# Kernel tuning notes

Hardware: AMD Instinct MI355X
Metric: run time of the kernel (lower is better)

## Reference

```python
import jax, jax.numpy as jnp
from jax import lax
import numpy as np

COMMITMENT_COST = 0.25
N_EMBED = 512
EDIM = 32


def _conv(x, w, b, stride, pad):
    # x: NCHW, w: OIHW (torch Conv2d layout)
    y = lax.conv_general_dilated(x, w, (stride, stride), [(pad, pad), (pad, pad)],
                                 dimension_numbers=("NCHW", "OIHW", "NCHW"))
    return y + b[None, :, None, None]


def _conv_t(x, w, b, stride, pad):
    # torch ConvTranspose2d weight layout: (in, out, kH, kW)
    k = w.shape[2]
    w_ = jnp.flip(w, (2, 3)).transpose(1, 0, 2, 3)  # -> OIHW
    p = k - 1 - pad
    y = lax.conv_general_dilated(x, w_, (1, 1), [(p, p), (p, p)],
                                 lhs_dilation=(stride, stride),
                                 dimension_numbers=("NCHW", "OIHW", "NCHW"))
    return y + b[None, :, None, None]


def setup_inputs() -> dict:
    key = jax.random.key(0)
    ks = jax.random.split(key, 9)
    rn = lambda k, s: jax.random.normal(k, s, jnp.float32) * 0.05
    return {
        "x": jax.random.normal(ks[0], (32, 3, 256, 256), jnp.float32),
        "e_w1": rn(ks[1], (64, 3, 4, 4)),    "e_b1": jnp.zeros((64,), jnp.float32),
        "e_w2": rn(ks[2], (128, 64, 4, 4)),  "e_b2": jnp.zeros((128,), jnp.float32),
        "e_w3": rn(ks[3], (32, 128, 3, 3)),  "e_b3": jnp.zeros((32,), jnp.float32),
        "embed": jax.random.uniform(ks[4], (N_EMBED, EDIM), jnp.float32,
                                    -1.0 / N_EMBED, 1.0 / N_EMBED),
        "d_w1": rn(ks[5], (32, 128, 3, 3)),  "d_b1": jnp.zeros((128,), jnp.float32),
        "d_w2": rn(ks[6], (128, 64, 4, 4)),  "d_b2": jnp.zeros((64,), jnp.float32),
        "d_w3": rn(ks[7], (64, 3, 4, 4)),    "d_b3": jnp.zeros((3,), jnp.float32),
    }


def reference(x, e_w1, e_b1, e_w2, e_b2, e_w3, e_b3, embed,
              d_w1, d_b1, d_w2, d_b2, d_w3, d_b3):
    # ---- encoder ----
    h = jax.nn.relu(_conv(x, e_w1, e_b1, 2, 1))   # [B,64,128,128]
    h = jax.nn.relu(_conv(h, e_w2, e_b2, 2, 1))   # [B,128,64,64]
    z = jax.nn.relu(_conv(h, e_w3, e_b3, 1, 1))   # [B,32,64,64]
    # ---- vector quantizer ----
    zp = z.transpose(0, 2, 3, 1)                  # BHWC
    zf = zp.reshape(-1, EDIM)                     # [N, 32]
    d = (zf ** 2).sum(1, keepdims=True) + (embed ** 2).sum(1) \
        - 2.0 * zf @ embed.T                      # [N, n_embed]
    idx = jnp.argmin(d, axis=1)                   # [N]
    z_q = embed[idx].reshape(zp.shape)            # gather == onehot @ embed
    sg = lax.stop_gradient
    loss = jnp.mean((sg(z_q) - zp) ** 2) + COMMITMENT_COST * jnp.mean((z_q - sg(zp)) ** 2)
    z_q_st = zp + sg(z_q - zp)                    # straight-through
    z_q_st = z_q_st.transpose(0, 3, 1, 2)         # back to NCHW
    # ---- decoder ----
    h = jax.nn.relu(_conv_t(z_q_st, d_w1, d_b1, 1, 1))  # [B,128,64,64]
    h = jax.nn.relu(_conv_t(h, d_w2, d_b2, 2, 1))       # [B,64,128,128]
    x_recon = _conv_t(h, d_w3, d_b3, 2, 1)              # [B,3,256,256]
    return x_recon, loss
```

## Files before the change

### kernel.cpp

```cpp
#include <hip/hip_runtime.h>


typedef __attribute__((ext_vector_type(8))) short     short8;
typedef __attribute__((ext_vector_type(4))) short     s16x4;
typedef __attribute__((ext_vector_type(8))) __bf16    bf16x8;
typedef __attribute__((ext_vector_type(4))) float     f32x4;
typedef __attribute__((ext_vector_type(4))) unsigned  uint32x4;

__device__ __forceinline__ float b2f(unsigned short b) {
  union { unsigned u; float f; } v; v.u = ((unsigned)b) << 16; return v.f;
}
__device__ __forceinline__ unsigned short f2b(float f) {
  union { float f; unsigned u; } v; v.f = f;
  unsigned r = v.u + 0x7FFF + ((v.u >> 16) & 1);
  return (unsigned short)(r >> 16);
}

__global__ __launch_bounds__(256) void prep1v_k(const float* __restrict__ w,
                                                unsigned short* __restrict__ wq) {
  const int i = blockIdx.x*256 + threadIdx.x;
  const int j = i & 7, l = (i >> 3) & 63, ni = (i >> 9) & 3, ks = i >> 11;
  const int k = ks*32 + (l >> 4)*8 + j;
  const int co = ni*16 + (l & 15);
  wq[i] = (k < 48) ? f2b(w[co*48 + k]) : (unsigned short)0;
}
__global__ __launch_bounds__(256) void prep2v_k(const float* __restrict__ w,
                                                unsigned short* __restrict__ wq) {
  const int i = blockIdx.x*256 + threadIdx.x;
  const int j = i & 7, l = (i >> 3) & 63, ni = (i >> 9) & 7, ks = i >> 12;
  const int lm = l & 15, lk = l >> 4;
  const int tap = ks >> 1, cc = ks & 1;
  const int co = ni*16 + lm, ci = cc*32 + lk*8 + j;
  wq[i] = f2b(w[(co*64 + ci)*16 + tap]);
}
__global__ __launch_bounds__(256) void prep3v_k(const float* __restrict__ w,
                                                unsigned short* __restrict__ wq) {
  const int i = blockIdx.x*256 + threadIdx.x;
  const int j = i & 7, l = (i >> 3) & 63, ni = (i >> 9) & 1, ks = i >> 10;
  const int lm = l & 15, lk = l >> 4;
  const int tap = ks >> 2, cf = ks & 3;
  const int co = ni*16 + lm, ci = cf*32 + lk*8 + j;
  wq[i] = f2b(w[(co*128 + ci)*9 + tap]);
}
__global__ __launch_bounds__(256) void prep4v_k(const float* __restrict__ w,
                                                unsigned short* __restrict__ wq) {
  const int i = blockIdx.x*256 + threadIdx.x;
  const int j = i & 7, l = (i >> 3) & 63, ni = (i >> 9) & 7, tap = i >> 12;
  const int lm = l & 15, lk = l >> 4;
  const int co = ni*16 + lm, ci = lk*8 + j;
  wq[i] = f2b(w[(ci*128 + co)*9 + (8 - tap)]);
}
__global__ __launch_bounds__(256) void prep5v_k(const float* __restrict__ w,
                                                unsigned short* __restrict__ wq) {
  const int i = blockIdx.x*256 + threadIdx.x;
  const int j = i & 7, l = (i >> 3) & 63, ni = (i >> 9) & 3;
  const int ks = (i >> 11) & 15, p = i >> 15;
  const int lm = l & 15, lk = l >> 4;
  const int py = p >> 1, px = p & 1;
  const int a = ks >> 3, b = (ks >> 2) & 1, cc = ks & 3;
  const int co = ni*16 + lm, ci = cc*32 + lk*8 + j;
  const int ky = 3 - 2*a - py, kx = 3 - 2*b - px;
  wq[i] = f2b(w[(ci*64 + co)*16 + ky*4 + kx]);
}
__global__ __launch_bounds__(256) void prep6_k(const float* __restrict__ w,
                                               unsigned short* __restrict__ wq) {
  const int i = blockIdx.x*256 + threadIdx.x;
  const int j = i & 7, l = (i >> 3) & 63, kc = (i >> 9) & 7, p = i >> 12;
  const int lm = l & 15, lk = l >> 4;
  const int a = kc >> 2, b = (kc >> 1) & 1, ch = kc & 1;
  const int ci = ch*32 + lk*8 + j, co = lm;
  const int py = p >> 1, px = p & 1;
  const int ky = 2 - 2*a + (1 - py), kx = 2 - 2*b + (1 - px);
  wq[i] = (co < 3) ? f2b(w[(ci*3 + co)*16 + ky*4 + kx]) : (unsigned short)0;
}

__global__ __launch_bounds__(256) void conv1m_k(const float* __restrict__ x,
    const unsigned short* __restrict__ wv, const float* __restrict__ bias,
    unsigned short* __restrict__ out) {
  __shared__ __align__(16) short RAW[12*264];
  __shared__ __align__(16) short IC[128*64];
  const int wid = ((blockIdx.x & 7) << 9) + (blockIdx.x >> 3);
  const int q = wid & 127, n = wid >> 7;
  for (int i = threadIdx.x; i < 396; i += 256)
    *(short8*)&RAW[i*8] = (short8)(short)0;
  __syncthreads();
  for (int s = threadIdx.x; s < 768; s += 256) {
    const int g = s >> 6, seg = s & 63;
    const int ci = g >> 2, ky = g & 3;
    const int iy = 2*q - 1 + ky;
    if (iy >= 0 && iy < 256) {
      const f32x4 v = *(const f32x4*)&x[((n*3 + ci)*256 + iy)*256 + seg*4];
      s16x4 sv;
      #pragma unroll
      for (int e = 0; e < 4; ++e) sv[e] = (short)f2b(v[e]);
      *(s16x4*)&RAW[g*264 + 4 + seg*4] = sv;
    }
  }
  __syncthreads();
  for (int s = threadIdx.x; s < 1024; s += 256) {
    const int kb = s & 7, ox = s >> 3;
    short8 v = (short8)(short)0;
    if (kb < 6) {
      const unsigned* u0 = (const unsigned*)&RAW[(2*kb  )*264 + 2*ox + 2];
      const unsigned* u1 = (const unsigned*)&RAW[(2*kb+1)*264 + 2*ox + 2];
      const unsigned a0 = u0[0], a1 = u0[1], a2 = u0[2];
      const unsigned b0 = u1[0], b1 = u1[1], b2 = u1[2];
      uint32x4 uv;
      uv[0] = (a0 >> 16) | (a1 << 16);
      uv[1] = (a1 >> 16) | (a2 << 16);
      uv[2] = (b0 >> 16) | (b1 << 16);
      uv[3] = (b1 >> 16) | (b2 << 16);
      v = __builtin_bit_cast(short8, uv);
    }
    const int bo = ((ox << 7) + (kb << 4)) ^ ((ox & 7) << 4);
    *(short8*)((char*)IC + bo) = v;
  }
  __syncthreads();
  const int w = threadIdx.x >> 6, l = threadIdx.x & 63;
  const int lm = l & 15, lk = l >> 4;
  f32x4 acc[2][4];
  #pragma unroll
  for (int mi = 0; mi < 2; ++mi)
    #pragma unroll
    for (int ni = 0; ni < 4; ++ni) acc[mi][ni] = (f32x4)0.0f;
  #pragma unroll
  for (int ks = 0; ks < 2; ++ks) {
    short8 bv[4];
    #pragma unroll
    for (int ni = 0; ni < 4; ++ni)
      bv[ni] = *(const short8*)(wv + (((ks*4 + ni)*64 + l) << 3));
    #pragma unroll
    for (int mi = 0; mi < 2; ++mi) {
      const int ox = w*32 + mi*16 + lm;
      const int bo = ((ox << 7) + (ks << 6) + (lk << 4)) ^ ((ox & 7) << 4);
      const short8 av = *(const short8*)((const char*)IC + bo);
      #pragma unroll
      for (int ni = 0; ni < 4; ++ni)
        acc[mi][ni] = __builtin_amdgcn_mfma_f32_16x16x32_bf16(
            __builtin_bit_cast(bf16x8, av),
            __builtin_bit_cast(bf16x8, bv[ni]),
            acc[mi][ni], 0, 0, 0);
    }
  }
  __syncthreads();
  #pragma unroll
  for (int mi = 0; mi < 2; ++mi)
    #pragma unroll
    for (int ni = 0; ni < 4; ++ni) {
      const int co = ni*16 + lm;
      const float bv = bias[co];
      #pragma unroll
      for (int r = 0; r < 4; ++r) {
        const int ox = w*32 + mi*16 + lk*4 + r;
        const int bo = ((ox << 7) + 2*co) ^ ((ox & 7) << 4);
        *(short*)((char*)IC + bo) = (short)f2b(fmaxf(acc[mi][ni][r] + bv, 0.f));
      }
    }
  __syncthreads();
  const long ob = ((long)(n*128 + q)) * 8192;
  for (int s = threadIdx.x; s < 1024; s += 256) {
    const int kb = s & 7, ox = s >> 3;
    const int bo = ((ox << 7) + (kb << 4)) ^ ((ox & 7) << 4);
    *(short8*)&out[ob + ox*64 + kb*8] = *(const short8*)((const char*)IC + bo);
  }
}

#define C2_LOAD(c) \
  _Pragma("unroll") \
  for (int s = 0; s < 9; ++s) { \
    st[s] = (short8)(short)0; \
    if (goff[s] >= 0) st[s] = *(const short8*)(in + goff[s] + (c)*32); \
  }
#define C2_WRITE \
  _Pragma("unroll") \
  for (int s = 0; s < 9; ++s) \
    if (lb[s] >= 0) *(short8*)((char*)IL + lb[s]) = st[s];
#define C2_COMPUTE(c) \
  _Pragma("unroll") \
  for (int t = 0; t < 16; ++t) { \
    const int ky = t >> 2, kx = t & 3; \
    const int p = 1 - (kx & 1), d = kx >> 1; \
    const short8 bv0 = *(const short8*)(wb + (t*2 + (c))*4096); \
    const short8 bv1 = *(const short8*)(wb + (t*2 + (c))*4096 + 512); \
    const char* Ab = (const char*)IL + (Bd0 + d*64); \
    const int imm0 = ((ky*2 + p)*66) << 6; \
    _Pragma("unroll") \
    for (int mi = 0; mi < 4; ++mi) { \
      const short8 av = *(const short8*)(Ab + imm0 + mi*1024); \
      acc[mi][0] = __builtin_amdgcn_mfma_f32_16x16x32_bf16( \
          __builtin_bit_cast(bf16x8, av), __builtin_bit_cast(bf16x8, bv0), \
          acc[mi][0], 0, 0, 0); \
      acc[mi][1] = __builtin_amdgcn_mfma_f32_16x16x32_bf16( \
          __builtin_bit_cast(bf16x8, av), __builtin_bit_cast(bf16x8, bv1), \
          acc[mi][1], 0, 0, 0); \
    } \
  }
__global__ __launch_bounds__(256) void conv2m_k(const unsigned short* __restrict__ in,
    const unsigned short* __restrict__ wv, const float* __restrict__ bias,
    unsigned short* __restrict__ out) {
  __shared__ short IL[8*66*32];
  const int wid = (blockIdx.x & 7)*256 + (blockIdx.x >> 3);
  const int q = wid & 63, n = wid >> 6;
  const int w = threadIdx.x >> 6, l = threadIdx.x & 63;
  const int lm = l & 15, lk = l >> 4;
  const int Bd0 = lm*64 + lk*16;
  const unsigned short* wb = wv + w*1024 + l*8;
  int goff[9], lb[9];
  #pragma unroll
  for (int s = 0; s < 9; ++s) {
    const int i = threadIdx.x + s*256;
    const int part = i & 3, e = i >> 2;
    const int idx = e % 66, rp = e / 66;
    const int r = rp >> 1, p = rp & 1;
    const int iy = 2*q - 1 + r, ix = 2*idx - p;
    const bool ok = (i < 2112) && iy >= 0 && iy < 128 && ix >= 0 && ix < 128;
    goff[s] = ok ? (((n*128 + iy)*128 + ix)*64 + part*8) : -1;
    lb[s]   = (i < 2112) ? (e*64 + part*16) : -1;
  }
  f32x4 acc[4][2];
  #pragma unroll
  for (int mi = 0; mi < 4; ++mi)
    #pragma unroll
    for (int ni = 0; ni < 2; ++ni) acc[mi][ni] = (f32x4)0.0f;
  short8 st[9];
  C2_LOAD(0); C2_WRITE;
  __syncthreads();
  C2_LOAD(1);
  C2_COMPUTE(0);
  __syncthreads();
  C2_WRITE;
  __syncthreads();
  C2_COMPUTE(1);
  #pragma unroll
  for (int mi = 0; mi < 4; ++mi)
    #pragma unroll
    for (int r = 0; r < 4; ++r) {
      const int ox = mi*16 + lk*4 + r;
      const int ob = ((n*64 + q)*64 + ox)*128;
      #pragma unroll
      for (int ni = 0; ni < 2; ++ni) {
        const int co = (w*2 + ni)*16 + lm;
        out[ob + co] = f2b(fmaxf(acc[mi][ni][r] + bias[co], 0.f));
      }
    }
}

#define C3_LOAD(c) \
  _Pragma("unroll") \
  for (int s = 0; s < 9; ++s) { \
    st[s] = (short8)(short)0; \
    if (goff[s] >= 0) st[s] = *(const short8*)(in + goff[s] + (c)*64); \
  }
#define C3_WRITE \
  _Pragma("unroll") \
  for (int s = 0; s < 9; ++s) \
    if (lb[s] >= 0) *(short8*)((char*)IL + lb[s]) = st[s];
#define C3_COMPUTE(c) \
  _Pragma("unroll") \
  for (int u = 0; u < 18; ++u) { \
    const int tap = u >> 1, cc = u & 1; \
    const int ky = tap / 3, kx = tap % 3; \
    const int ks = tap*4 + (c)*2 + cc; \
    const short8 bv0 = *(const short8*)(wb + ks*1024); \
    const short8 bv1 = *(const short8*)(wb + ks*1024 + 512); \
    const char* Ab = (const char*)IL + (Wc[kx][cc]); \
    const int imm0 = ky*8448; \
    _Pragma("unroll") \
    for (int mi = 0; mi < 2; ++mi) { \
      const short8 av = *(const short8*)(Ab + imm0 + mi*2048); \
      acc[mi][0] = __builtin_amdgcn_mfma_f32_16x16x32_bf16( \
          __builtin_bit_cast(bf16x8, av), __builtin_bit_cast(bf16x8, bv0), \
          acc[mi][0], 0, 0, 0); \
      acc[mi][1] = __builtin_amdgcn_mfma_f32_16x16x32_bf16( \
          __builtin_bit_cast(bf16x8, av), __builtin_bit_cast(bf16x8, bv1), \
          acc[mi][1], 0, 0, 0); \
    } \
  }
__global__ __launch_bounds__(256) void conv3m_k(const unsigned short* __restrict__ in,
    const unsigned short* __restrict__ wv, const float* __restrict__ bias,
    float* __restrict__ out) {
  __shared__ short IL[4*66*64];
  const int wid = (blockIdx.x & 7)*128 + (blockIdx.x >> 3);
  const int q = wid & 31, n = wid >> 5;
  const int w = threadIdx.x >> 6, l = threadIdx.x & 63;
  const int lm = l & 15, lk = l >> 4;
  const int row = w >> 1, oxb = (w & 1) * 32;
  int goff[9], lb[9];
  #pragma unroll
  for (int s = 0; s < 9; ++s) {
    const int i = threadIdx.x + s*256;
    const int part = i & 7, e = i >> 3;
    const int col = e % 66, r = e / 66;
    const int iy = 2*q - 1 + r, ix = col - 1;
    const bool ok = (i < 2112) && iy >= 0 && iy < 64 && ix >= 0 && ix < 64;
    goff[s] = ok ? (((n*64 + iy)*64 + ix)*128 + part*8) : -1;
    lb[s]   = (i < 2112) ? ((e << 7) + ((part << 4) ^ ((col & 7) << 4))) : -1;
  }
  int Wc[3][2];
  #pragma unroll
  for (int kx = 0; kx < 3; ++kx) {
    const int e = oxb + lm + kx;
    Wc[kx][0] = row*8448 + (e << 7) + ((lk << 4) ^ ((e & 7) << 4));
    Wc[kx][1] = Wc[kx][0] ^ 0x40;
  }
  const unsigned short* wb = wv + l*8;
  f32x4 acc[2][2];
  #pragma unroll
  for (int mi = 0; mi < 2; ++mi)
    #pragma unroll
    for (int ni = 0; ni < 2; ++ni) acc[mi][ni] = (f32x4)0.0f;
  short8 st[9];
  C3_LOAD(0); C3_WRITE;
  __syncthreads();
  C3_LOAD(1);
  C3_COMPUTE(0);
  __syncthreads();
  C3_WRITE;
  __syncthreads();
  C3_COMPUTE(1);
  const int oy = 2*q + row;
  #pragma unroll
  for (int mi = 0; mi < 2; ++mi)
    #pragma unroll
    for (int r = 0; r < 4; ++r) {
      const int ox = oxb + mi*16 + lk*4 + r;
      const long mb = ((long)((n*64 + oy)*64 + ox)) * 32;
      #pragma unroll
      for (int ni = 0; ni < 2; ++ni) {
        const int co = ni*16 + lm;
        out[mb + co] = fmaxf(acc[mi][ni][r] + bias[co], 0.f);
      }
    }
}

__global__ __launch_bounds__(256) void d1m_k(const float* __restrict__ in,
    const unsigned short* __restrict__ wv, const float* __restrict__ bias,
    unsigned short* __restrict__ out) {
  __shared__ short IL[264*40];
  const int wid = (blockIdx.x & 7)*128 + (blockIdx.x >> 3);
  const int q = wid & 31, n = wid >> 5;
  const int w = threadIdx.x >> 6, l = threadIdx.x & 63;
  const int lm = l & 15, lk = l >> 4;
  const int row = w >> 1, oxb = (w & 1) * 32;
  for (int i = threadIdx.x; i < 1056; i += 256) {
    const int part = i & 3, e = i >> 2;
    const int col = e % 66, r = e / 66;
    const int iy = 2*q - 1 + r, ix = col - 1;
    short8 v = (short8)(short)0;
    if (iy >= 0 && iy < 64 && ix >= 0 && ix < 64) {
      const float* p = in + (((long)((n*64 + iy)*64 + ix)) * 32 + part*8);
      const f32x4 f0 = *(const f32x4*)p;
      const f32x4 f1 = *(const f32x4*)(p + 4);
      #pragma unroll
      for (int e2 = 0; e2 < 4; ++e2) {
        v[e2]     = (short)f2b(f0[e2]);
        v[e2 + 4] = (short)f2b(f1[e2]);
      }
    }
    *(short8*)&IL[e*40 + part*8] = v;
  }
  const unsigned short* wb = wv + l*8;
  int Wd[3];
  #pragma unroll
  for (int kx = 0; kx < 3; ++kx)
    Wd[kx] = row*5280 + (oxb + lm + kx)*80 + lk*16;
  __syncthreads();
  f32x4 acc[2][8];
  #pragma unroll
  for (int mi = 0; mi < 2; ++mi)
    #pragma unroll
    for (int ni = 0; ni < 8; ++ni) acc[mi][ni] = (f32x4)0.0f;
  #pragma unroll
  for (int tap = 0; tap < 9; ++tap) {
    const int ky = tap / 3, kx = tap % 3;
    short8 bv[8];
    #pragma unroll
    for (int ni = 0; ni < 8; ++ni)
      bv[ni] = *(const short8*)(wb + (tap*8 + ni)*512);
    const char* Ab = (const char*)IL + Wd[kx];
    const int imm0 = ky*5280;
    #pragma unroll
    for (int mi = 0; mi < 2; ++mi) {
      const short8 av = *(const short8*)(Ab + imm0 + mi*1280);
      #pragma unroll
      for (int ni = 0; ni < 8; ++ni)
        acc[mi][ni] = __builtin_amdgcn_mfma_f32_16x16x32_bf16(
            __builtin_bit_cast(bf16x8, av),
            __builtin_bit_cast(bf16x8, bv[ni]),
            acc[mi][ni], 0, 0, 0);
    }
  }
  const int oy = 2*q + row;
  #pragma unroll
  for (int mi = 0; mi < 2; ++mi)
    #pragma unroll
    for (int r = 0; r < 4; ++r) {
      const int ox = oxb + mi*16 + lk*4 + r;
      const int ob = ((n*64 + oy)*64 + ox)*128;
      #pragma unroll
      for (int ni = 0; ni < 8; ++ni) {
        const int co = ni*16 + lm;
        out[ob + co] = f2b(fmaxf(acc[mi][ni][r] + bias[co], 0.f));
      }
    }
}

#define CT2_LOAD(c) \
  _Pragma("unroll") \
  for (int s = 0; s < 7; ++s) { \
    st[s] = (short8)(short)0; \
    if (goff[s] >= 0) st[s] = *(const short8*)(in + goff[s] + (c)*64); \
  }
#define CT2_WRITE \
  _Pragma("unroll") \
  for (int s = 0; s < 7; ++s) \
    if (lb[s] >= 0) *(short8*)((char*)IL + lb[s]) = st[s];
#define CT2_COMPUTE(c) \
  _Pragma("unroll") \
  for (int u = 0; u < 8; ++u) { \
    const int a = u >> 2, b = (u >> 1) & 1, c1 = u & 1; \
    const int ks = (a << 3) | (b << 2) | (2*(c) + c1); \
    short8 bv[4]; \
    _Pragma("unroll") \
    for (int ni = 0; ni < 4; ++ni) \
      bv[ni] = *(const short8*)(wb + ks*2048 + ni*512); \
    const char* Ab = (const char*)IL + (pyb + Wb[b][c1]); \
    const int imm0 = a*8448; \
    _Pragma("unroll") \
    for (int mi = 0; mi < 4; ++mi) { \
      const short8 av = *(const short8*)(Ab + imm0 + mi*2048); \
      _Pragma("unroll") \
      for (int ni = 0; ni < 4; ++ni) \
        acc[mi][ni] = __builtin_amdgcn_mfma_f32_16x16x32_bf16( \
            __builtin_bit_cast(bf16x8, av), \
            __builtin_bit_cast(bf16x8, bv[ni]), \
            acc[mi][ni], 0, 0, 0); \
    } \
  }
__global__ __launch_bounds__(256) void convt2m_k(const unsigned short* __restrict__ in,
    const unsigned short* __restrict__ wv, const float* __restrict__ bias,
    unsigned short* __restrict__ out) {
  __shared__ short IL[3*66*64];
  const int wid = (blockIdx.x & 7)*256 + (blockIdx.x >> 3);
  const int q = wid & 63, n = wid >> 6;
  const int w = threadIdx.x >> 6, l = threadIdx.x & 63;
  const int py = w >> 1, px = w & 1;
  const int lm = l & 15, lk = l >> 4;
  int Wb[2][2];
  #pragma unroll
  for (int b = 0; b < 2; ++b) {
    const int e = lm + px + b;
    Wb[b][0] = (e << 7) + ((lk << 4) ^ ((e & 7) << 4));
    Wb[b][1] = Wb[b][0] ^ 0x40;
  }
  const int pyb = py * 8448;
  const unsigned short* wb = wv + w*32768 + l*8;
  int goff[7], lb[7];
  #pragma unroll
  for (int s = 0; s < 7; ++s) {
    const int i = threadIdx.x + s*256;
    const int part = i & 7, e = i >> 3;
    const int col = e % 66, r = e / 66;
    const int iy = q - 1 + r, ix = col - 1;
    const bool ok = (i < 1584) && iy >= 0 && iy < 64 && ix >= 0 && ix < 64;
    goff[s] = ok ? (((n*64 + iy)*64 + ix)*128 + part*8) : -1;
    lb[s]   = (i < 1584) ? ((e << 7) + ((part << 4) ^ ((col & 7) << 4))) : -1;
  }
  f32x4 acc[4][4];
  #pragma unroll
  for (int mi = 0; mi < 4; ++mi)
    #pragma unroll
    for (int ni = 0; ni < 4; ++ni) acc[mi][ni] = (f32x4)0.0f;
  short8 st[7];
  CT2_LOAD(0); CT2_WRITE;
  __syncthreads();
  CT2_LOAD(1);
  CT2_COMPUTE(0);
  __syncthreads();
  CT2_WRITE;
  __syncthreads();
  CT2_COMPUTE(1);
  const int oy = 2*q + py;
  #pragma unroll
  for (int mi = 0; mi < 4; ++mi)
    #pragma unroll
    for (int r = 0; r < 4; ++r) {
      const int ox = 2*(mi*16 + lk*4 + r) + px;
      const int ob = ((n*128 + oy)*128 + ox)*64;
      #pragma unroll
      for (int ni = 0; ni < 4; ++ni) {
        const int co = ni*16 + lm;
        out[ob + co] = f2b(fmaxf(acc[mi][ni][r] + bias[co], 0.f));
      }
    }
}

__global__ __launch_bounds__(256) void vqm_k(const float* __restrict__ z,
    const float* __restrict__ embed, float* __restrict__ zq,
    float* __restrict__ partial) {
  __shared__ short Be[512*40];
  __shared__ float en[512];
  __shared__ int   bidx[128];
  __shared__ float red[256];
  const int m0 = blockIdx.x * 128;
  for (int i = threadIdx.x; i < 4096; i += 256) {
    const int j = i >> 3, k0 = (i & 7) * 4;
    const f32x4 v = *(const f32x4*)&embed[j*32 + k0];
    s16x4 s;
    #pragma unroll
    for (int e = 0; e < 4; ++e) s[e] = (short)f2b(v[e]);
    *(s16x4*)&Be[j*40 + k0] = s;
  }
  __syncthreads();
  for (int j = threadIdx.x; j < 512; j += 256) {
    float s = 0.f;
    #pragma unroll
    for (int q = 0; q < 4; ++q) {
      const short8 v = *(const short8*)&Be[j*40 + q*8];
      #pragma unroll
      for (int e = 0; e < 8; ++e) {
        const float f = b2f((unsigned short)v[e]);
        s = fmaf(f, f, s);
      }
    }
    en[j] = s;
  }
  __syncthreads();
  const int w = threadIdx.x >> 6, l = threadIdx.x & 63;
  const int lm = l & 15, lk = l >> 4;
  const int rw = w * 32;
  short8 av[2];
  #pragma unroll
  for (int mi = 0; mi < 2; ++mi) {
    const float* zp = z + (long)(m0 + rw + mi*16 + lm)*32 + lk*8;
    const f32x4 f0 = *(const f32x4*)zp;
    const f32x4 f1 = *(const f32x4*)(zp + 4);
    short8 v;
    #pragma unroll
    for (int e = 0; e < 4; ++e) {
      v[e]     = (short)f2b(f0[e]);
      v[e + 4] = (short)f2b(f1[e]);
    }
    av[mi] = v;
  }
  float bd[2][4]; int bj[2][4];
  #pragma unroll
  for (int mi = 0; mi < 2; ++mi)
    #pragma unroll
    for (int r = 0; r < 4; ++r) { bd[mi][r] = 1e30f; bj[mi][r] = 0; }
  for (int nc = 0; nc < 8; ++nc) {
    f32x4 acc[2][4];
    #pragma unroll
    for (int mi = 0; mi < 2; ++mi)
      #pragma unroll
      for (int ni = 0; ni < 4; ++ni) acc[mi][ni] = (f32x4)0.0f;
    #pragma unroll
    for (int ni = 0; ni < 4; ++ni) {
      const short8 bv = *(const short8*)&Be[(nc*64 + ni*16 + lm)*40 + lk*8];
      #pragma unroll
      for (int mi = 0; mi < 2; ++mi)
        acc[mi][ni] = __builtin_amdgcn_mfma_f32_16x16x32_bf16(
            __builtin_bit_cast(bf16x8, av[mi]),
            __builtin_bit_cast(bf16x8, bv),
            acc[mi][ni], 0, 0, 0);
    }
    #pragma unroll
    for (int ni = 0; ni < 4; ++ni) {
      const int j = nc*64 + ni*16 + lm;
      const float e_n = en[j];
      #pragma unroll
      for (int mi = 0; mi < 2; ++mi)
        #pragma unroll
        for (int r = 0; r < 4; ++r) {
          const float d = fmaf(-2.f, acc[mi][ni][r], e_n);
          if (d < bd[mi][r]) { bd[mi][r] = d; bj[mi][r] = j; }
        }
    }
  }
  #pragma unroll
  for (int mi = 0; mi < 2; ++mi)
    #pragma unroll
    for (int r = 0; r < 4; ++r) {
      float d = bd[mi][r]; int j = bj[mi][r];
      #pragma unroll
      for (int off = 1; off < 16; off <<= 1) {
        const float od = __shfl_xor(d, off);
        const int   oj = __shfl_xor(j, off);
        if (od < d || (od == d && oj < j)) { d = od; j = oj; }
      }
      if (lm == 0) bidx[rw + mi*16 + lk*4 + r] = j;
    }
  __syncthreads();
  const int pl = threadIdx.x >> 1, hf = (threadIdx.x & 1) * 16;
  const int code = bidx[pl];
  const long pb = (long)(m0 + pl)*32 + hf;
  float se = 0.f;
  #pragma unroll
  for (int q = 0; q < 4; ++q) {
    const f32x4 ev = *(const f32x4*)&embed[code*32 + hf + q*4];
    const f32x4 zv = *(const f32x4*)&z[pb + q*4];
    *(f32x4*)&zq[pb + q*4] = ev;
    const f32x4 df = ev - zv;
    #pragma unroll
    for (int e = 0; e < 4; ++e) se = fmaf(df[e], df[e], se);
  }
  red[threadIdx.x] = se; __syncthreads();
  for (int s = 128; s > 0; s >>= 1) {
    if (threadIdx.x < s) red[threadIdx.x] += red[threadIdx.x + s];
    __syncthreads();
  }
  if (threadIdx.x == 0) partial[blockIdx.x] = red[0];
}

__global__ __launch_bounds__(256) void loss_k(const float* __restrict__ part,
                                              float* __restrict__ out) {
  __shared__ float red[256];
  const int t = threadIdx.x;
  float s = 0.f;
  #pragma unroll
  for (int q = 0; q < 4; ++q) s += part[t + q*256];
  red[t] = s; __syncthreads();
  for (int st = 128; st > 0; st >>= 1) {
    if (t < st) red[t] += red[t + st];
    __syncthreads();
  }
  if (t == 0) out[0] = red[0] * (1.25f / (131072.f * 32.f));
}

__global__ __launch_bounds__(256) void convt3m_k(const unsigned short* __restrict__ in,
    const unsigned short* __restrict__ wq6, const float* __restrict__ bias,
    float* __restrict__ out) {
  __shared__ short8 IL[3*8*66];
  const int h = blockIdx.x & 1, q = (blockIdx.x >> 1) & 127, n = blockIdx.x >> 8;
  for (int i = threadIdx.x; i < 1584; i += 256) {
    const int c8 = i & 7, t = i >> 3, ixl = t % 66, r = t / 66;
    const int iy = q - 1 + r, ix = h*64 - 1 + ixl;
    short8 v = (short8)(short)0;
    if (iy >= 0 && iy < 128 && ix >= 0 && ix < 128)
      v = *(const short8*)(in + (((long)(n*128 + iy)*128 + ix)*64 + c8*8));
    IL[(r*8 + c8)*66 + ixl] = v;
  }
  const int w = threadIdx.x >> 6, l = threadIdx.x & 63;
  const int py = w >> 1, px = w & 1;
  const int lm = l & 15, lk = l >> 4;
  short8 bfrag[8];
  #pragma unroll
  for (int kc = 0; kc < 8; ++kc)
    bfrag[kc] = *(const short8*)(wq6 + (((w*8 + kc)*64 + l) << 3));
  __syncthreads();
  f32x4 acc[4];
  #pragma unroll
  for (int mi = 0; mi < 4; ++mi) acc[mi] = (f32x4)0.0f;
  #pragma unroll
  for (int kc = 0; kc < 8; ++kc) {
    const int a = kc >> 2, b = (kc >> 1) & 1, ch = kc & 1;
    const int base = (((py + a)*8 + ch*4 + lk)*66) + px + b;
    #pragma unroll
    for (int mi = 0; mi < 4; ++mi) {
      const short8 av = *(const short8*)&IL[base + mi*16 + lm];
      acc[mi] = __builtin_amdgcn_mfma_f32_16x16x32_bf16(
          __builtin_bit_cast(bf16x8, av),
          __builtin_bit_cast(bf16x8, bfrag[kc]),
          acc[mi], 0, 0, 0);
    }
  }
  if (lm < 3) {
    const float bv = bias[lm];
    const int oy = 2*q + py;
    const long ob = ((long)(n*3 + lm))*65536 + oy*256;
    #pragma unroll
    for (int mi = 0; mi < 4; ++mi)
      #pragma unroll
      for (int r = 0; r < 4; ++r) {
        const int xq = mi*16 + lk*4 + r;
        out[ob + h*128 + 2*xq + px] = acc[mi][r] + bv;
      }
  }
}

extern "C" void kernel_launch(void* const* d_in, const int* in_sizes, int n_in,
                              void* d_out, int out_size, void* d_ws, size_t ws_size,
                              hipStream_t stream) {
  const float* x   = (const float*)d_in[0];
  const float* ew1 = (const float*)d_in[1];  const float* eb1 = (const float*)d_in[2];
  const float* ew2 = (const float*)d_in[3];  const float* eb2 = (const float*)d_in[4];
  const float* ew3 = (const float*)d_in[5];  const float* eb3 = (const float*)d_in[6];
  const float* emb = (const float*)d_in[7];
  const float* dw1 = (const float*)d_in[8];  const float* db1 = (const float*)d_in[9];
  const float* dw2 = (const float*)d_in[10]; const float* db2 = (const float*)d_in[11];
  const float* dw3 = (const float*)d_in[12]; const float* db3 = (const float*)d_in[13];
  float* out = (float*)d_out;

  uint8_t* w8 = (uint8_t*)d_ws;
  unsigned short* h1 = (unsigned short*)w8;
  unsigned short* h2 = (unsigned short*)(w8 + 67108864);
  float* z   = (float*)(w8 + 100663296);
  float* zq  = (float*)(w8 + 117440512);
  float* part = (float*)(w8 + 67108864);
  unsigned short* wq2 = (unsigned short*)(w8 + 117440512);
  unsigned short* wq3 = (unsigned short*)(w8 + 117440512 + 262144);
  unsigned short* wq1 = (unsigned short*)(w8 + 117440512 + 335872);
  unsigned short* wq4 = (unsigned short*)(w8 + 100663296);
  unsigned short* wq5 = (unsigned short*)(w8 + 100663296 + 73728);
  unsigned short* wq6 = (unsigned short*)(w8 + 100663296 + 335872);
  unsigned short* d1 = h2;
  unsigned short* d2 = h1;

  prep1v_k<<<dim3(16),256,0,stream>>>(ew1, wq1);
  prep2v_k<<<dim3(512),256,0,stream>>>(ew2, wq2);
  prep3v_k<<<dim3(144),256,0,stream>>>(ew3, wq3);
  conv1m_k<<<dim3(4096),256,0,stream>>>(x, wq1, eb1, h1);
  conv2m_k<<<dim3(2048),256,0,stream>>>(h1, wq2, eb2, h2);
  conv3m_k<<<dim3(1024),256,0,stream>>>(h2, wq3, eb3, z);
  vqm_k<<<dim3(1024),256,0,stream>>>(z, emb, zq, part);
  loss_k<<<dim3(1),256,0,stream>>>(part, out + 6291456);
  prep4v_k<<<dim3(144),256,0,stream>>>(dw1, wq4);
  prep5v_k<<<dim3(512),256,0,stream>>>(dw2, wq5);
  prep6_k<<<dim3(64),256,0,stream>>>(dw3, wq6);
  d1m_k<<<dim3(1024),256,0,stream>>>(zq, wq4, db1, d1);
  convt2m_k<<<dim3(2048),256,0,stream>>>(d1, wq5, db2, d2);
  convt3m_k<<<dim3(8192),256,0,stream>>>(d2, wq6, db3, out);
}
```

Measured before the change: 358.7 us.

## Fuse vector quantizer into conv3 epilogue and precompute codebook fragments

The VQ argmin, codebook gather and loss partial sums now run inside the conv3 kernel on its output tile, staged through shared memory. This removes the fp32 z round trip to global memory and one kernel launch. A new prep kernel pre-packs the bf16 codebook into MFMA fragment order and computes codebook norms once, instead of every VQ block doing this. All weight prep kernels are moved ahead of the convolutions and the workspace layout is rearranged to fit. The cost is more shared-memory reuse and registers in conv3, which may lower its occupancy.

```diff
diff --git a/kernel.cpp b/kernel.cpp
--- a/kernel.cpp
+++ b/kernel.cpp
@@ -72,6 +72,22 @@
   const int py = p >> 1, px = p & 1;
   const int ky = 2 - 2*a + (1 - py), kx = 2 - 2*b + (1 - px);
   wq[i] = (co < 3) ? f2b(w[(ci*3 + co)*16 + ky*4 + kx]) : (unsigned short)0;
+}
+__global__ __launch_bounds__(256) void prepe_k(const float* __restrict__ emb,
+    unsigned short* __restrict__ wqe, float* __restrict__ en) {
+  const int i = blockIdx.x*256 + threadIdx.x;
+  const int j = i & 7, l = (i >> 3) & 63, ni = (i >> 9) & 3, nc = i >> 11;
+  const int lm = l & 15, lk = l >> 4;
+  wqe[i] = f2b(emb[(nc*64 + ni*16 + lm)*32 + lk*8 + j]);
+  if (i < 512) {
+    float s = 0.f;
+    #pragma unroll
+    for (int k = 0; k < 32; ++k) {
+      const float f = b2f(f2b(emb[i*32 + k]));
+      s = fmaf(f, f, s);
+    }
+    en[i] = s;
+  }
 }
 
 __global__ __launch_bounds__(256) void conv1m_k(const float* __restrict__ x,
@@ -276,9 +292,11 @@
           acc[mi][1], 0, 0, 0); \
     } \
   }
-__global__ __launch_bounds__(256) void conv3m_k(const unsigned short* __restrict__ in,
+__global__ __launch_bounds__(256) void conv3v_k(const unsigned short* __restrict__ in,
     const unsigned short* __restrict__ wv, const float* __restrict__ bias,
-    float* __restrict__ out) {
+    const unsigned short* __restrict__ wqe, const float* __restrict__ eng,
+    const float* __restrict__ emb, float* __restrict__ zq,
+    float* __restrict__ part) {
   __shared__ short IL[4*66*64];
   const int wid = (blockIdx.x & 7)*128 + (blockIdx.x >> 3);
   const int q = wid & 31, n = wid >> 5;
@@ -289,12 +307,12 @@
   #pragma unroll
   for (int s = 0; s < 9; ++s) {
     const int i = threadIdx.x + s*256;
-    const int part = i & 7, e = i >> 3;
+    const int part_ = i & 7, e = i >> 3;
     const int col = e % 66, r = e / 66;
     const int iy = 2*q - 1 + r, ix = col - 1;
     const bool ok = (i < 2112) && iy >= 0 && iy < 64 && ix >= 0 && ix < 64;
-    goff[s] = ok ? (((n*64 + iy)*64 + ix)*128 + part*8) : -1;
-    lb[s]   = (i < 2112) ? ((e << 7) + ((part << 4) ^ ((col & 7) << 4))) : -1;
+    goff[s] = ok ? (((n*64 + iy)*64 + ix)*128 + part_*8) : -1;
+    lb[s]   = (i < 2112) ? ((e << 7) + ((part_ << 4) ^ ((col & 7) << 4))) : -1;
   }
   int Wc[3][2];
   #pragma unroll
@@ -318,19 +336,98 @@
   C3_WRITE;
   __syncthreads();
   C3_COMPUTE(1);
-  const int oy = 2*q + row;
+  __syncthreads();
+  short* ZB  = (short*)IL;
+  float* ZF  = (float*)((char*)IL + 10240);
+  int*  bidx = (int*)((char*)IL + 28672);
+  float* red = (float*)((char*)IL + 29184);
+  #pragma unroll
+  for (int mi = 0; mi < 2; ++mi)
+    #pragma unroll
+    for (int ni = 0; ni < 2; ++ni) {
+      const int co = ni*16 + lm;
+      const float bv = bias[co];
+      #pragma unroll
+      for (int r = 0; r < 4; ++r) {
+        const int pos = row*64 + oxb + mi*16 + lk*4 + r;
+        const float v = fmaxf(acc[mi][ni][r] + bv, 0.f);
+        ZB[pos*40 + co] = (short)f2b(v);
+        ZF[pos*36 + co] = v;
+      }
+    }
+  __syncthreads();
+  short8 av[2];
+  #pragma unroll
+  for (int mi = 0; mi < 2; ++mi)
+    av[mi] = *(const short8*)&ZB[(row*64 + oxb + mi*16 + lm)*40 + lk*8];
+  float bd[2][4]; int bj[2][4];
+  #pragma unroll
+  for (int mi = 0; mi < 2; ++mi)
+    #pragma unroll
+    for (int r = 0; r < 4; ++r) { bd[mi][r] = 1e30f; bj[mi][r] = 0; }
+  for (int nc = 0; nc < 8; ++nc) {
+    f32x4 a2[2][4];
+    #pragma unroll
+    for (int mi = 0; mi < 2; ++mi)
+      #pragma unroll
+      for (int ni = 0; ni < 4; ++ni) a2[mi][ni] = (f32x4)0.0f;
+    #pragma unroll
+    for (int ni = 0; ni < 4; ++ni) {
+      const short8 bv = *(const short8*)(wqe + (((nc*4 + ni)*64 + l) << 3));
+      #pragma unroll
+      for (int mi = 0; mi < 2; ++mi)
+        a2[mi][ni] = __builtin_amdgcn_mfma_f32_16x16x32_bf16(
+            __builtin_bit_cast(bf16x8, av[mi]),
+            __builtin_bit_cast(bf16x8, bv),
+            a2[mi][ni], 0, 0, 0);
+    }
+    #pragma unroll
+    for (int ni = 0; ni < 4; ++ni) {
+      const int j = nc*64 + ni*16 + lm;
+      const float e_n = eng[j];
+      #pragma unroll
+      for (int mi = 0; mi < 2; ++mi)
+        #pragma unroll
+        for (int r = 0; r < 4; ++r) {
+          const float d = fmaf(-2.f, a2[mi][ni][r], e_n);
+          if (d < bd[mi][r]) { bd[mi][r] = d; bj[mi][r] = j; }
+        }
+    }
+  }
   #pragma unroll
   for (int mi = 0; mi < 2; ++mi)
     #pragma unroll
     for (int r = 0; r < 4; ++r) {
-      const int ox = oxb + mi*16 + lk*4 + r;
-      const long mb = ((long)((n*64 + oy)*64 + ox)) * 32;
-      #pragma unroll
-      for (int ni = 0; ni < 2; ++ni) {
-        const int co = ni*16 + lm;
-        out[mb + co] = fmaxf(acc[mi][ni][r] + bias[co], 0.f);
+      float d = bd[mi][r]; int j = bj[mi][r];
+      #pragma unroll
+      for (int off = 1; off < 16; off <<= 1) {
+        const float od = __shfl_xor(d, off);
+        const int   oj = __shfl_xor(j, off);
+        if (od < d || (od == d && oj < j)) { d = od; j = oj; }
       }
-    }
+      if (lm == 0) bidx[row*64 + oxb + mi*16 + lk*4 + r] = j;
+    }
+  __syncthreads();
+  const int pl = threadIdx.x >> 1, hf = (threadIdx.x & 1) * 16;
+  const int code = bidx[pl];
+  const int oy2 = 2*q + (pl >> 6), ox2 = pl & 63;
+  const long zqo = ((long)((n*64 + oy2)*64 + ox2)) * 32 + hf;
+  float se = 0.f;
+  #pragma unroll
+  for (int qq = 0; qq < 4; ++qq) {
+    const f32x4 ev = *(const f32x4*)&emb[code*32 + hf + qq*4];
+    const f32x4 zv = *(const f32x4*)&ZF[pl*36 + hf + qq*4];
+    *(f32x4*)&zq[zqo + qq*4] = ev;
+    const f32x4 df = ev - zv;
+    #pragma unroll
+    for (int e = 0; e < 4; ++e) se = fmaf(df[e], df[e], se);
+  }
+  red[threadIdx.x] = se; __syncthreads();
+  for (int s2 = 128; s2 > 0; s2 >>= 1) {
+    if (threadIdx.x < s2) red[threadIdx.x] += red[threadIdx.x + s2];
+    __syncthreads();
+  }
+  if (threadIdx.x == 0) part[blockIdx.x] = red[0];
 }
 
 __global__ __launch_bounds__(256) void d1m_k(const float* __restrict__ in,
@@ -495,123 +592,6 @@
     }
 }
 
-__global__ __launch_bounds__(256) void vqm_k(const float* __restrict__ z,
-    const float* __restrict__ embed, float* __restrict__ zq,
-    float* __restrict__ partial) {
-  __shared__ short Be[512*40];
-  __shared__ float en[512];
-  __shared__ int   bidx[128];
-  __shared__ float red[256];
-  const int m0 = blockIdx.x * 128;
-  for (int i = threadIdx.x; i < 4096; i += 256) {
-    const int j = i >> 3, k0 = (i & 7) * 4;
-    const f32x4 v = *(const f32x4*)&embed[j*32 + k0];
-    s16x4 s;
-    #pragma unroll
-    for (int e = 0; e < 4; ++e) s[e] = (short)f2b(v[e]);
-    *(s16x4*)&Be[j*40 + k0] = s;
-  }
-  __syncthreads();
-  for (int j = threadIdx.x; j < 512; j += 256) {
-    float s = 0.f;
-    #pragma unroll
-    for (int q = 0; q < 4; ++q) {
-      const short8 v = *(const short8*)&Be[j*40 + q*8];
-      #pragma unroll
-      for (int e = 0; e < 8; ++e) {
-        const float f = b2f((unsigned short)v[e]);
-        s = fmaf(f, f, s);
-      }
-    }
-    en[j] = s;
-  }
-  __syncthreads();
-  const int w = threadIdx.x >> 6, l = threadIdx.x & 63;
-  const int lm = l & 15, lk = l >> 4;
-  const int rw = w * 32;
-  short8 av[2];
-  #pragma unroll
-  for (int mi = 0; mi < 2; ++mi) {
-    const float* zp = z + (long)(m0 + rw + mi*16 + lm)*32 + lk*8;
-    const f32x4 f0 = *(const f32x4*)zp;
-    const f32x4 f1 = *(const f32x4*)(zp + 4);
-    short8 v;
-    #pragma unroll
-    for (int e = 0; e < 4; ++e) {
-      v[e]     = (short)f2b(f0[e]);
-      v[e + 4] = (short)f2b(f1[e]);
-    }
-    av[mi] = v;
-  }
-  float bd[2][4]; int bj[2][4];
-  #pragma unroll
-  for (int mi = 0; mi < 2; ++mi)
-    #pragma unroll
-    for (int r = 0; r < 4; ++r) { bd[mi][r] = 1e30f; bj[mi][r] = 0; }
-  for (int nc = 0; nc < 8; ++nc) {
-    f32x4 acc[2][4];
-    #pragma unroll
-    for (int mi = 0; mi < 2; ++mi)
-      #pragma unroll
-      for (int ni = 0; ni < 4; ++ni) acc[mi][ni] = (f32x4)0.0f;
-    #pragma unroll
-    for (int ni = 0; ni < 4; ++ni) {
-      const short8 bv = *(const short8*)&Be[(nc*64 + ni*16 + lm)*40 + lk*8];
-      #pragma unroll
-      for (int mi = 0; mi < 2; ++mi)
-        acc[mi][ni] = __builtin_amdgcn_mfma_f32_16x16x32_bf16(
-            __builtin_bit_cast(bf16x8, av[mi]),
-            __builtin_bit_cast(bf16x8, bv),
-            acc[mi][ni], 0, 0, 0);
-    }
-    #pragma unroll
-    for (int ni = 0; ni < 4; ++ni) {
-      const int j = nc*64 + ni*16 + lm;
-      const float e_n = en[j];
-      #pragma unroll
-      for (int mi = 0; mi < 2; ++mi)
-        #pragma unroll
-        for (int r = 0; r < 4; ++r) {
-          const float d = fmaf(-2.f, acc[mi][ni][r], e_n);
-          if (d < bd[mi][r]) { bd[mi][r] = d; bj[mi][r] = j; }
-        }
-    }
-  }
-  #pragma unroll
-  for (int mi = 0; mi < 2; ++mi)
-    #pragma unroll
-    for (int r = 0; r < 4; ++r) {
-      float d = bd[mi][r]; int j = bj[mi][r];
-      #pragma unroll
-      for (int off = 1; off < 16; off <<= 1) {
-        const float od = __shfl_xor(d, off);
-        const int   oj = __shfl_xor(j, off);
-        if (od < d || (od == d && oj < j)) { d = od; j = oj; }
-      }
-      if (lm == 0) bidx[rw + mi*16 + lk*4 + r] = j;
-    }
-  __syncthreads();
-  const int pl = threadIdx.x >> 1, hf = (threadIdx.x & 1) * 16;
-  const int code = bidx[pl];
-  const long pb = (long)(m0 + pl)*32 + hf;
-  float se = 0.f;
-  #pragma unroll
-  for (int q = 0; q < 4; ++q) {
-    const f32x4 ev = *(const f32x4*)&embed[code*32 + hf + q*4];
-    const f32x4 zv = *(const f32x4*)&z[pb + q*4];
-    *(f32x4*)&zq[pb + q*4] = ev;
-    const f32x4 df = ev - zv;
-    #pragma unroll
-    for (int e = 0; e < 4; ++e) se = fmaf(df[e], df[e], se);
-  }
-  red[threadIdx.x] = se; __syncthreads();
-  for (int s = 128; s > 0; s >>= 1) {
-    if (threadIdx.x < s) red[threadIdx.x] += red[threadIdx.x + s];
-    __syncthreads();
-  }
-  if (threadIdx.x == 0) partial[blockIdx.x] = red[0];
-}
-
 __global__ __launch_bounds__(256) void loss_k(const float* __restrict__ part,
                                               float* __restrict__ out) {
   __shared__ float red[256];
@@ -694,29 +674,31 @@
   uint8_t* w8 = (uint8_t*)d_ws;
   unsigned short* h1 = (unsigned short*)w8;
   unsigned short* h2 = (unsigned short*)(w8 + 67108864);
-  float* z   = (float*)(w8 + 100663296);
+  uint8_t* zr = w8 + 100663296;
   float* zq  = (float*)(w8 + 117440512);
-  float* part = (float*)(w8 + 67108864);
+  unsigned short* wqe = (unsigned short*)zr;
+  float* eng = (float*)(zr + 32768);
+  float* part = (float*)(zr + 36864);
+  unsigned short* wq3 = (unsigned short*)(zr + 40960);
+  unsigned short* wq4 = (unsigned short*)(zr + 131072);
+  unsigned short* wq5 = (unsigned short*)(zr + 262144);
+  unsigned short* wq6 = (unsigned short*)(zr + 524288);
   unsigned short* wq2 = (unsigned short*)(w8 + 117440512);
-  unsigned short* wq3 = (unsigned short*)(w8 + 117440512 + 262144);
   unsigned short* wq1 = (unsigned short*)(w8 + 117440512 + 335872);
-  unsigned short* wq4 = (unsigned short*)(w8 + 100663296);
-  unsigned short* wq5 = (unsigned short*)(w8 + 100663296 + 73728);
-  unsigned short* wq6 = (unsigned short*)(w8 + 100663296 + 335872);
   unsigned short* d1 = h2;
   unsigned short* d2 = h1;
 
+  prepe_k<<<dim3(64),256,0,stream>>>(emb, wqe, eng);
   prep1v_k<<<dim3(16),256,0,stream>>>(ew1, wq1);
   prep2v_k<<<dim3(512),256,0,stream>>>(ew2, wq2);
   prep3v_k<<<dim3(144),256,0,stream>>>(ew3, wq3);
-  conv1m_k<<<dim3(4096),256,0,stream>>>(x, wq1, eb1, h1);
-  conv2m_k<<<dim3(2048),256,0,stream>>>(h1, wq2, eb2, h2);
-  conv3m_k<<<dim3(1024),256,0,stream>>>(h2, wq3, eb3, z);
-  vqm_k<<<dim3(1024),256,0,stream>>>(z, emb, zq, part);
-  loss_k<<<dim3(1),256,0,stream>>>(part, out + 6291456);
   prep4v_k<<<dim3(144),256,0,stream>>>(dw1, wq4);
   prep5v_k<<<dim3(512),256,0,stream>>>(dw2, wq5);
   prep6_k<<<dim3(64),256,0,stream>>>(dw3, wq6);
+  conv1m_k<<<dim3(4096),256,0,stream>>>(x, wq1, eb1, h1);
+  conv2m_k<<<dim3(2048),256,0,stream>>>(h1, wq2, eb2, h2);
+  conv3v_k<<<dim3(1024),256,0,stream>>>(h2, wq3, eb3, wqe, eng, emb, zq, part);
+  loss_k<<<dim3(1),256,0,stream>>>(part, out + 6291456);
   d1m_k<<<dim3(1024),256,0,stream>>>(zq, wq4, db1, d1);
   convt2m_k<<<dim3(2048),256,0,stream>>>(d1, wq5, db2, d2);
   convt3m_k<<<dim3(8192),256,0,stream>>>(d2, wq6, db3, out);
```

After: 355.8 us. Within noise of the previous version (-0.8%).
